# Kernel tuning notes

Hardware: AMD Instinct MI355X
Metric: run time of the kernel (lower is better)

## Reference

```python
import jax, jax.numpy as jnp
import numpy as np

B, N, F = 32, 1024, 128

def setup_inputs() -> dict:
    key = jax.random.key(0)
    k1, k2, k3, k4 = jax.random.split(key, 4)
    adjMs = jax.random.uniform(k1, (B, N, N), dtype=jnp.float32)
    feats = jax.random.normal(k2, (B, N, F), dtype=jnp.float32)
    w = jax.random.normal(k3, (F, F), dtype=jnp.float32) * 0.05  # random_normal init scale
    b = jax.random.normal(k4, (1,), dtype=jnp.float32)
    return {"adjMs": adjMs, "feats": feats, "w": w, "b": b}

def reference(adjMs, feats, w, b):
    # adj[b,i,j] = feats[b,i] @ w @ feats[b,j] + b  (bilinear form V W V^T + b)
    vw = jnp.einsum('bnf,fg->bng', feats, w)          # [B,N,F]
    y = jnp.einsum('bng,bmg->bnm', vw, feats) + b[0]  # [B,N,N]
    # activation = 'linear' (identity); invertProb=False so no inversion branch
    return (y, feats)
```

## Files before the change

### kernel.cpp

```cpp
#include <hip/hip_runtime.h>

#define Bsz 32
#define Nn  1024
#define Ff  128

typedef __attribute__((ext_vector_type(8))) short bf16x8;
typedef __attribute__((ext_vector_type(4))) float f32x4;

static __device__ inline short f2bf(float f) {
    unsigned u = __builtin_bit_cast(unsigned, f);
    unsigned r = u + 0x7FFFu + ((u >> 16) & 1u);
    return (short)(r >> 16);
}
static __device__ inline unsigned pack2(float lo, float hi) {
    return (unsigned)(unsigned short)f2bf(lo) | ((unsigned)(unsigned short)f2bf(hi) << 16);
}

__global__ __launch_bounds__(256) void k1_fused_wt(
    const float* __restrict__ feats,
    const float* __restrict__ w,
    float* __restrict__ out_feats,
    short* __restrict__ fb,
    short* __restrict__ vw)
{
    __shared__ short wT_lds[128 * 128];

    const int tid  = threadIdx.x;
    const int wid  = tid >> 6;
    const int lane = tid & 63;
    const int lr = lane & 15;
    const int kg = lane >> 4;

    {
        const int g    = tid >> 1;
        const int kb   = (tid & 1) * 64;
        const int swzg = (g & 7) << 4;
        const size_t gofs = (size_t)g;
        for (int kk = 0; kk < 64; kk += 2) {
            int k = kb + kk;
            float lo = w[(size_t)k * Ff + gofs];
            float hi = w[(size_t)(k + 1) * Ff + gofs];
            unsigned pk = pack2(lo, hi);
            *(unsigned*)((char*)wT_lds + (g << 8) + ((k * 2) ^ swzg)) = pk;
        }
    }

    const int row0  = blockIdx.x * 64;
    const int myrow = row0 + wid * 16 + lr;
    const float* frow = feats + (size_t)myrow * Ff;
    float* orow       = out_feats + (size_t)myrow * Ff;
    short* brow       = fb + (size_t)myrow * Ff;

    bf16x8 a[4];
    for (int kc = 0; kc < 4; ++kc) {
        int k0 = kc * 32 + kg * 8;
        f32x4 v0 = ((const f32x4*)(frow + k0))[0];
        f32x4 v1 = ((const f32x4*)(frow + k0))[1];
        __builtin_nontemporal_store(v0, (f32x4*)(orow + k0));
        __builtin_nontemporal_store(v1, (f32x4*)(orow + k0) + 1);
        a[kc] = (bf16x8){ f2bf(v0[0]), f2bf(v0[1]), f2bf(v0[2]), f2bf(v0[3]),
                          f2bf(v1[0]), f2bf(v1[1]), f2bf(v1[2]), f2bf(v1[3]) };
        *((bf16x8*)(brow + k0)) = a[kc];
    }
    __syncthreads();

    f32x4 acc[8] = {};
    const int swz = (lr & 7) << 4;
    for (int kc = 0; kc < 4; ++kc) {
        const int kbyte = kc * 64 + kg * 16;
        for (int nf = 0; nf < 8; ++nf) {
            const int row = nf * 16 + lr;
            bf16x8 b = *(const bf16x8*)((char*)wT_lds + (row << 8) + (kbyte ^ swz));
            acc[nf] = __builtin_amdgcn_mfma_f32_16x16x32_bf16(a[kc], b, acc[nf], 0, 0, 0);
        }
    }

    for (int nf = 0; nf < 8; ++nf) {
        int g = nf * 16 + lr;
        for (int r = 0; r < 4; ++r)
            vw[(size_t)(row0 + wid * 16 + kg * 4 + r) * Ff + g] = f2bf(acc[nf][r]);
    }
}

__global__ __launch_bounds__(256, 4) void gemm2_kernel(
    const short* __restrict__ vw,
    const short* __restrict__ fb,
    const float* __restrict__ bias,
    float* __restrict__ y)
{
    __shared__ float tbuf[4][2][16 * 68];

    int blk   = blockIdx.x;
    int xcd   = blk & 7;
    int q     = blk >> 3;
    int chunk = q >> 4;
    int k     = q & 15;
    int super_id = chunk * 8 + xcd;
    int bidx  = super_id >> 2;
    int s     = super_id & 3;
    int sm = s >> 1, sn = s & 1;
    int mt = sm * 4 + (k >> 2);
    int nt = sn * 4 + (k & 3);

    int tid = threadIdx.x;
    int wid = tid >> 6, lane = tid & 63;
    int wm = wid >> 1, wn = wid & 1;
    int lr = lane & 15, kg = lane >> 4;

    const short* A  = vw + (size_t)bidx * Nn * Ff;
    const short* Bp = fb + (size_t)bidx * Nn * Ff;
    int am0 = mt * 128 + wm * 64;
    int bn0 = nt * 128 + wn * 64;

    const float bv = bias[0];

    f32x4 acc[4][4] = {};

    for (int kc = 0; kc < 4; ++kc) {
        int k0 = kc * 32 + kg * 8;
        bf16x8 b[4];
        for (int nf = 0; nf < 4; ++nf)
            b[nf] = *((const bf16x8*)(Bp + (size_t)(bn0 + nf * 16 + lr) * Ff + k0));
        for (int mf = 0; mf < 4; ++mf) {
            bf16x8 a = *((const bf16x8*)(A + (size_t)(am0 + mf * 16 + lr) * Ff + k0));
            for (int nf = 0; nf < 4; ++nf)
                acc[mf][nf] = __builtin_amdgcn_mfma_f32_16x16x32_bf16(
                    a, b[nf], acc[mf][nf], 0, 0, 0);
        }
    }

    float* Y = y + (size_t)bidx * Nn * Nn;
    const int c4 = lr * 4;

    for (int mf = 0; mf < 4; ++mf) {
        float* L = tbuf[wid][mf & 1];
        for (int nf = 0; nf < 4; ++nf)
            for (int r = 0; r < 4; ++r)
                L[(kg * 4 + r) * 68 + nf * 16 + lr] = acc[mf][nf][r] + bv;
        __threadfence_block();
        for (int rg = 0; rg < 4; ++rg) {
            int rl = rg * 4 + kg;
            f32x4 v = *((const f32x4*)&L[rl * 68 + c4]);
            __builtin_nontemporal_store(
                v, (f32x4*)(Y + (size_t)(am0 + mf * 16 + rl) * Nn + bn0 + c4));
        }
    }
}

extern "C" void kernel_launch(void* const* d_in, const int* in_sizes, int n_in,
                              void* d_out, int out_size, void* d_ws, size_t ws_size,
                              hipStream_t stream) {
    const float* feats = (const float*)d_in[1];
    const float* w     = (const float*)d_in[2];
    const float* bias  = (const float*)d_in[3];
    float* y = (float*)d_out;
    float* out_feats = y + (size_t)Bsz * Nn * Nn;

    short* vw = (short*)d_ws;
    short* fb = vw + (size_t)Bsz * Nn * Ff;

    k1_fused_wt<<<512, 256, 0, stream>>>(feats, w, out_feats, fb, vw);
    gemm2_kernel<<<2048, 256, 0, stream>>>(vw, fb, bias, y);
}
```

Before: 55.79 us.

## Retile GEMM2 so each block computes full 16-row strips across all columns

The second GEMM now gives each block one 16-row strip of a batch, with each of its four waves covering 256 columns (16 MFMA tiles sharing a single A fragment), in place of 128x128 tiles. Block-to-batch mapping is changed so each XCD handles four whole batches. The epilogue stages rows through a padded 262-float LDS buffer so each wave writes 1 KB contiguous row segments with nontemporal stores. The aim is longer contiguous output writes and simpler indexing, at the cost of much less B reuse per block, since each B fragment now feeds only one MFMA and B traffic from L2 rises.

```diff
diff --git a/kernel.cpp b/kernel.cpp
--- a/kernel.cpp
+++ b/kernel.cpp
@@ -88,62 +88,53 @@
     const float* __restrict__ bias,
     float* __restrict__ y)
 {
-    __shared__ float tbuf[4][2][16 * 68];
+    __shared__ float tbuf[4][8 * 262];
 
-    int blk   = blockIdx.x;
-    int xcd   = blk & 7;
-    int q     = blk >> 3;
-    int chunk = q >> 4;
-    int k     = q & 15;
-    int super_id = chunk * 8 + xcd;
-    int bidx  = super_id >> 2;
-    int s     = super_id & 3;
-    int sm = s >> 1, sn = s & 1;
-    int mt = sm * 4 + (k >> 2);
-    int nt = sn * 4 + (k & 3);
+    int blk  = blockIdx.x;
+    int xcd  = blk & 7;
+    int q    = blk >> 3;
+    int bidx = xcd * 4 + (q >> 6);
+    int rg   = q & 63;
 
     int tid = threadIdx.x;
     int wid = tid >> 6, lane = tid & 63;
-    int wm = wid >> 1, wn = wid & 1;
     int lr = lane & 15, kg = lane >> 4;
+    int cb = wid * 256;
 
-    const short* A  = vw + (size_t)bidx * Nn * Ff;
+    const short* A  = vw + ((size_t)bidx * Nn + rg * 16 + lr) * Ff;
     const short* Bp = fb + (size_t)bidx * Nn * Ff;
-    int am0 = mt * 128 + wm * 64;
-    int bn0 = nt * 128 + wn * 64;
 
-    const float bv = bias[0];
-
-    f32x4 acc[4][4] = {};
+    f32x4 acc[16] = {};
 
     for (int kc = 0; kc < 4; ++kc) {
         int k0 = kc * 32 + kg * 8;
-        bf16x8 b[4];
-        for (int nf = 0; nf < 4; ++nf)
-            b[nf] = *((const bf16x8*)(Bp + (size_t)(bn0 + nf * 16 + lr) * Ff + k0));
-        for (int mf = 0; mf < 4; ++mf) {
-            bf16x8 a = *((const bf16x8*)(A + (size_t)(am0 + mf * 16 + lr) * Ff + k0));
-            for (int nf = 0; nf < 4; ++nf)
-                acc[mf][nf] = __builtin_amdgcn_mfma_f32_16x16x32_bf16(
-                    a, b[nf], acc[mf][nf], 0, 0, 0);
+        bf16x8 a = *((const bf16x8*)(A + k0));
+        for (int nf = 0; nf < 16; ++nf) {
+            bf16x8 b = *((const bf16x8*)(Bp + (size_t)(cb + nf * 16 + lr) * Ff + k0));
+            acc[nf] = __builtin_amdgcn_mfma_f32_16x16x32_bf16(a, b, acc[nf], 0, 0, 0);
         }
     }
 
-    float* Y = y + (size_t)bidx * Nn * Nn;
-    const int c4 = lr * 4;
+    const float bv = bias[0];
+    float* Yr = y + ((size_t)bidx * Nn + rg * 16) * Nn;
+    float* L  = tbuf[wid];
 
-    for (int mf = 0; mf < 4; ++mf) {
-        float* L = tbuf[wid][mf & 1];
-        for (int nf = 0; nf < 4; ++nf)
-            for (int r = 0; r < 4; ++r)
-                L[(kg * 4 + r) * 68 + nf * 16 + lr] = acc[mf][nf][r] + bv;
+    for (int h = 0; h < 2; ++h) {
+        for (int rr2 = 0; rr2 < 2; ++rr2) {
+            int r = h * 2 + rr2;
+            int s = kg * 2 + rr2;
+            for (int nf = 0; nf < 16; ++nf)
+                L[s * 262 + nf * 16 + lr] = acc[nf][r] + bv;
+        }
         __threadfence_block();
-        for (int rg = 0; rg < 4; ++rg) {
-            int rl = rg * 4 + kg;
-            f32x4 v = *((const f32x4*)&L[rl * 68 + c4]);
+        for (int i = 0; i < 8; ++i) {
+            int rr = (i >> 1) * 4 + h * 2 + (i & 1);
+            int s  = (i >> 1) * 2 + (i & 1);
+            f32x4 v = *((const f32x4*)&L[s * 262 + lane * 4]);
             __builtin_nontemporal_store(
-                v, (f32x4*)(Y + (size_t)(am0 + mf * 16 + rl) * Nn + bn0 + c4));
+                v, (f32x4*)(Yr + (size_t)rr * Nn + cb + lane * 4));
         }
+        __threadfence_block();
     }
 }
 
```

Measured after the change: 91.59 us. 64.2% more time.
